# Kernel optimization log

Hardware: AMD Instinct MI355X
Metric: run time of the kernel (lower is better)

The kernel has to match this reference:

```python
import jax, jax.numpy as jnp
import numpy as np

SEGMENTS = 64
SU2NDIM = 16
N = 16  # SU(2^4) matrix dimension
BATCH = 128


def setup_inputs() -> dict:
    key = jax.random.key(0)
    # Small scale keeps expm well-conditioned (skew-ish generators in practice)
    x = 0.1 * jax.random.normal(key, (BATCH, SEGMENTS * SU2NDIM, N, N), dtype=jnp.float32)
    return {"x": x}


def _batched_expm(a):
    # a: [..., N, N] -> expm over last two dims
    flat = a.reshape((-1, N, N))
    ex = jax.vmap(jax.scipy.linalg.expm)(flat)
    return ex.reshape(a.shape)


def reference(x):
    # maintensor = expm(-x), reversed along axis 0 (faithful to source)
    m = _batched_expm(-x)            # [B, S*D, N, N]
    m = m[::-1]                      # tf.reverse(maintensor, [0])
    b = m.shape[0]
    # tf.split along axis 1 into SEGMENTS contiguous chunks of SU2NDIM
    m = m.reshape(b, SEGMENTS, SU2NDIM, N, N)
    # Sequential chain product per segment: U = M[D-1] @ ... @ M[1] @ M[0] @ I
    ms = jnp.moveaxis(m, 2, 0)       # [D, B, S, N, N]
    u0 = jnp.broadcast_to(jnp.eye(N, dtype=x.dtype), (b, SEGMENTS, N, N))
    def step(u, mj):
        return mj @ u, None
    u, _ = jax.lax.scan(step, u0, ms)
    return u                         # [B, SEGMENTS, N, N] == transpose([1,0,2,3]) of stacked list
```

## Files before the change

kernel.cpp:

```cpp
#include <hip/hip_runtime.h>

typedef float f32x4 __attribute__((ext_vector_type(4)));
typedef short s16x8 __attribute__((ext_vector_type(8)));
typedef unsigned int uint;
typedef uint u32x4 __attribute__((ext_vector_type(4)));

union Frag {
  u32x4 u;
  s16x8 s;
};

__device__ __forceinline__ uint packhi(float f0, float f1) {
  uint a = __float_as_uint(f0) + 0x8000u;
  uint b = __float_as_uint(f1) + 0x8000u;
  return __builtin_amdgcn_perm(b, a, 0x07060302u);
}

__device__ __forceinline__ void split2(float f0, float f1, uint& hi, uint& lo) {
  uint a0 = __float_as_uint(f0) + 0x8000u;
  uint a1 = __float_as_uint(f1) + 0x8000u;
  hi = __builtin_amdgcn_perm(a1, a0, 0x07060302u);
  float h0 = __uint_as_float(a0 & 0xFFFF0000u);
  float h1 = __uint_as_float(a1 & 0xFFFF0000u);
  lo = packhi(f0 - h0, f1 - h1);
}

#define CFENCE() __asm__ __volatile__("" ::: "memory")

__device__ __forceinline__ f32x4 expm_negT(const float* __restrict__ A,
                                           uint* __restrict__ hb, int lo,
                                           int g, int gt, bool low, f32x4 idm) {
  float c0 = A[(8 * gt + 0) * 16 + lo], c1 = A[(8 * gt + 1) * 16 + lo];
  float c2 = A[(8 * gt + 2) * 16 + lo], c3 = A[(8 * gt + 3) * 16 + lo];
  float c4 = A[(8 * gt + 4) * 16 + lo], c5 = A[(8 * gt + 5) * 16 + lo];
  float c6 = A[(8 * gt + 6) * 16 + lo], c7 = A[(8 * gt + 7) * 16 + lo];
  f32x4 xr = *(const f32x4*)(A + lo * 16 + 4 * g);
  uint h, lw;
  Frag xa;
  split2(c0, c1, h, lw); xa.u[0] = low ? h : lw;
  split2(c2, c3, h, lw); xa.u[1] = low ? h : lw;
  split2(c4, c5, h, lw); xa.u[2] = low ? h : lw;
  split2(c6, c7, h, lw); xa.u[3] = low ? h : lw;
  f32x4 t;
#pragma unroll
  for (int i = 0; i < 4; ++i)
    t[i] = fmaf(1.f / 720.f, xr[i], (-1.f / 120.f) * idm[i]);
  const float SK[5] = {1.f / 24.f, -1.f / 6.f, 0.5f, -1.f, 1.f};
  uint* wp = hb + lo * 12 + 2 * g;
  const uint* rp = hb + lo * 12 + 4 * gt;
#pragma unroll
  for (int k = 0; k < 5; ++k) {
    wp[0] = packhi(t[0], t[1]);
    wp[1] = packhi(t[2], t[3]);
    CFENCE();
    Frag tb;
    tb.u = *(const u32x4*)rp;
    CFENCE();
    f32x4 acc = idm * SK[k];
    t = __builtin_amdgcn_mfma_f32_16x16x32_bf16(xa.s, tb.s, acc, 0, 0, 0);
  }
  return t;
}

__global__ __launch_bounds__(256, 8) void unitary_kernel(
    const float* __restrict__ x, float* __restrict__ out) {
  __shared__ uint HB[4][192];
  __shared__ uint PE[4][320];
  __shared__ uint PU[4][320];

  const int tid = threadIdx.x;
  const int w = tid >> 6;
  const int l = tid & 63;
  const int lo = l & 15;
  const int g = l >> 4;
  const int gt = g & 1;
  const bool low = g < 2;

  uint* hb = HB[w];
  uint* pe = PE[w];
  uint* pu = PU[w];

  const int ch = blockIdx.x * 4 + w;
  const float* xb =
      x + ((size_t)(127 - (ch >> 6)) * 1024 + (size_t)(ch & 63) * 16) * 256;

  f32x4 idm;
  idm[0] = (4 * g + 0 == lo) ? 1.f : 0.f;
  idm[1] = (4 * g + 1 == lo) ? 1.f : 0.f;
  idm[2] = (4 * g + 2 == lo) ? 1.f : 0.f;
  idm[3] = (4 * g + 3 == lo) ? 1.f : 0.f;

  Frag ifr;
  {
    uint v = ((lo >> 3) == gt) ? (0x3F80u << (16 * (lo & 1))) : 0u;
    int slot = (lo >> 1) & 3;
    ifr.u[0] = (slot == 0) ? v : 0u;
    ifr.u[1] = (slot == 1) ? v : 0u;
    ifr.u[2] = (slot == 2) ? v : 0u;
    ifr.u[3] = (slot == 3) ? v : 0u;
  }

  uint* pew = pe + lo * 20 + 4 * g;
  const uint* pea = pe + lo * 20 + 8 * gt + (low ? 0 : 2);
  uint* puw = pu + lo * 20 + 4 * g;
  const uint* pub = pu + lo * 20 + 8 * gt;

  f32x4 uc;
#pragma unroll 1
  for (int j = 0; j < 16; ++j) {
    f32x4 et = expm_negT(xb + j * 256, hb, lo, g, gt, low, idm);
    uint h0, l0, h1, l1;
    split2(et[0], et[1], h0, l0);
    split2(et[2], et[3], h1, l1);
    *(u32x4*)pew = (u32x4){h0, h1, l0, l1};
    if (j) {
      split2(uc[0], uc[1], h0, l0);
      split2(uc[2], uc[3], h1, l1);
      *(u32x4*)puw = (u32x4){h0, h1, l0, l1};
    }
    CFENCE();
    Frag ea;
    ea.u[0] = pea[0];
    ea.u[1] = pea[1];
    ea.u[2] = pea[4];
    ea.u[3] = pea[5];
    f32x4 z = {0.f, 0.f, 0.f, 0.f};
    if (j) {
      Frag b1, b2;
      b1.u[0] = pub[0];
      b1.u[1] = pub[1];
      b1.u[2] = pub[4];
      b1.u[3] = pub[5];
      b2.u[0] = pub[2];
      b2.u[1] = pub[3];
      b2.u[2] = pub[6];
      b2.u[3] = pub[7];
      CFENCE();
      f32x4 t1 = __builtin_amdgcn_mfma_f32_16x16x32_bf16(ea.s, b1.s, z, 0, 0, 0);
      uc = __builtin_amdgcn_mfma_f32_16x16x32_bf16(ea.s, b2.s, t1, 0, 0, 0);
    } else {
      CFENCE();
      uc = __builtin_amdgcn_mfma_f32_16x16x32_bf16(ea.s, ifr.s, z, 0, 0, 0);
    }
  }

  float* op = out + (size_t)ch * 256;
  op[(4 * g + 0) * 16 + lo] = uc[0];
  op[(4 * g + 1) * 16 + lo] = uc[1];
  op[(4 * g + 2) * 16 + lo] = uc[2];
  op[(4 * g + 3) * 16 + lo] = uc[3];
}

extern "C" void kernel_launch(void* const* d_in, const int* in_sizes, int n_in,
                              void* d_out, int out_size, void* d_ws,
                              size_t ws_size, hipStream_t stream) {
  const float* x = (const float*)d_in[0];
  float* out = (float*)d_out;
  unitary_kernel<<<dim3(2048), dim3(256), 0, stream>>>(x, out);
}
```

Baseline: 190.6 us.

## Batch four independent Taylor expm evaluations per wave to overlap MFMA chains

Restructures the per-wave loop to compute four matrix exponentials at once in groups, interleaving their Horner MFMA steps so independent MFMAs and LDS round-trips can overlap rather than serialize. It also drops the bf16 low-part split of the generator in expm (its low half is now zeros), which lowers precision. Shared memory grows to per-matrix staging buffers, and occupancy is lowered to 4 blocks per SM, trading latency hiding across waves for instruction-level parallelism within a wave.

```diff
diff --git a/kernel.cpp b/kernel.cpp
--- a/kernel.cpp
+++ b/kernel.cpp
@@ -3,6 +3,7 @@
 typedef float f32x4 __attribute__((ext_vector_type(4)));
 typedef short s16x8 __attribute__((ext_vector_type(8)));
 typedef unsigned int uint;
+typedef uint u32x2 __attribute__((ext_vector_type(2)));
 typedef uint u32x4 __attribute__((ext_vector_type(4)));
 
 union Frag {
@@ -16,57 +17,21 @@
   return __builtin_amdgcn_perm(b, a, 0x07060302u);
 }
 
-__device__ __forceinline__ void split2(float f0, float f1, uint& hi, uint& lo) {
+__device__ __forceinline__ void split2(float f0, float f1, uint& hi, uint& lw) {
   uint a0 = __float_as_uint(f0) + 0x8000u;
   uint a1 = __float_as_uint(f1) + 0x8000u;
   hi = __builtin_amdgcn_perm(a1, a0, 0x07060302u);
   float h0 = __uint_as_float(a0 & 0xFFFF0000u);
   float h1 = __uint_as_float(a1 & 0xFFFF0000u);
-  lo = packhi(f0 - h0, f1 - h1);
+  lw = packhi(f0 - h0, f1 - h1);
 }
 
 #define CFENCE() __asm__ __volatile__("" ::: "memory")
 
-__device__ __forceinline__ f32x4 expm_negT(const float* __restrict__ A,
-                                           uint* __restrict__ hb, int lo,
-                                           int g, int gt, bool low, f32x4 idm) {
-  float c0 = A[(8 * gt + 0) * 16 + lo], c1 = A[(8 * gt + 1) * 16 + lo];
-  float c2 = A[(8 * gt + 2) * 16 + lo], c3 = A[(8 * gt + 3) * 16 + lo];
-  float c4 = A[(8 * gt + 4) * 16 + lo], c5 = A[(8 * gt + 5) * 16 + lo];
-  float c6 = A[(8 * gt + 6) * 16 + lo], c7 = A[(8 * gt + 7) * 16 + lo];
-  f32x4 xr = *(const f32x4*)(A + lo * 16 + 4 * g);
-  uint h, lw;
-  Frag xa;
-  split2(c0, c1, h, lw); xa.u[0] = low ? h : lw;
-  split2(c2, c3, h, lw); xa.u[1] = low ? h : lw;
-  split2(c4, c5, h, lw); xa.u[2] = low ? h : lw;
-  split2(c6, c7, h, lw); xa.u[3] = low ? h : lw;
-  f32x4 t;
-#pragma unroll
-  for (int i = 0; i < 4; ++i)
-    t[i] = fmaf(1.f / 720.f, xr[i], (-1.f / 120.f) * idm[i]);
-  const float SK[5] = {1.f / 24.f, -1.f / 6.f, 0.5f, -1.f, 1.f};
-  uint* wp = hb + lo * 12 + 2 * g;
-  const uint* rp = hb + lo * 12 + 4 * gt;
-#pragma unroll
-  for (int k = 0; k < 5; ++k) {
-    wp[0] = packhi(t[0], t[1]);
-    wp[1] = packhi(t[2], t[3]);
-    CFENCE();
-    Frag tb;
-    tb.u = *(const u32x4*)rp;
-    CFENCE();
-    f32x4 acc = idm * SK[k];
-    t = __builtin_amdgcn_mfma_f32_16x16x32_bf16(xa.s, tb.s, acc, 0, 0, 0);
-  }
-  return t;
-}
-
-__global__ __launch_bounds__(256, 8) void unitary_kernel(
+__global__ __launch_bounds__(256, 4) void unitary_kernel(
     const float* __restrict__ x, float* __restrict__ out) {
-  __shared__ uint HB[4][192];
-  __shared__ uint PE[4][320];
-  __shared__ uint PU[4][320];
+  __shared__ uint TBH[4][4][192];
+  __shared__ uint TBL[4][4][192];
 
   const int tid = threadIdx.x;
   const int w = tid >> 6;
@@ -76,11 +41,7 @@
   const int gt = g & 1;
   const bool low = g < 2;
 
-  uint* hb = HB[w];
-  uint* pe = PE[w];
-  uint* pu = PU[w];
-
-  const int ch = blockIdx.x * 4 + w;
+  const int ch = __builtin_amdgcn_readfirstlane(blockIdx.x * 4 + w);
   const float* xb =
       x + ((size_t)(127 - (ch >> 6)) * 1024 + (size_t)(ch & 63) * 16) * 256;
 
@@ -90,57 +51,98 @@
   idm[2] = (4 * g + 2 == lo) ? 1.f : 0.f;
   idm[3] = (4 * g + 3 == lo) ? 1.f : 0.f;
 
-  Frag ifr;
-  {
-    uint v = ((lo >> 3) == gt) ? (0x3F80u << (16 * (lo & 1))) : 0u;
-    int slot = (lo >> 1) & 3;
-    ifr.u[0] = (slot == 0) ? v : 0u;
-    ifr.u[1] = (slot == 1) ? v : 0u;
-    ifr.u[2] = (slot == 2) ? v : 0u;
-    ifr.u[3] = (slot == 3) ? v : 0u;
-  }
-
-  uint* pew = pe + lo * 20 + 4 * g;
-  const uint* pea = pe + lo * 20 + 8 * gt + (low ? 0 : 2);
-  uint* puw = pu + lo * 20 + 4 * g;
-  const uint* pub = pu + lo * 20 + 8 * gt;
+  const int wb = lo * 12 + 2 * g;
+  const int rbB = lo * 12 + 4 * gt;
 
   f32x4 uc;
+
 #pragma unroll 1
-  for (int j = 0; j < 16; ++j) {
-    f32x4 et = expm_negT(xb + j * 256, hb, lo, g, gt, low, idm);
-    uint h0, l0, h1, l1;
-    split2(et[0], et[1], h0, l0);
-    split2(et[2], et[3], h1, l1);
-    *(u32x4*)pew = (u32x4){h0, h1, l0, l1};
-    if (j) {
-      split2(uc[0], uc[1], h0, l0);
-      split2(uc[2], uc[3], h1, l1);
-      *(u32x4*)puw = (u32x4){h0, h1, l0, l1};
+  for (int grp = 0; grp < 4; ++grp) {
+    const float* xg = xb + (size_t)grp * 1024;
+    Frag xa[4];
+    f32x4 t[4];
+#pragma unroll
+    for (int m = 0; m < 4; ++m) {
+      const float* A = xg + m * 256;
+      float c0 = A[(8 * gt + 0) * 16 + lo], c1 = A[(8 * gt + 1) * 16 + lo];
+      float c2 = A[(8 * gt + 2) * 16 + lo], c3 = A[(8 * gt + 3) * 16 + lo];
+      float c4 = A[(8 * gt + 4) * 16 + lo], c5 = A[(8 * gt + 5) * 16 + lo];
+      float c6 = A[(8 * gt + 6) * 16 + lo], c7 = A[(8 * gt + 7) * 16 + lo];
+      f32x4 xr = *(const f32x4*)(A + lo * 16 + 4 * g);
+      xa[m].u[0] = low ? packhi(c0, c1) : 0u;
+      xa[m].u[1] = low ? packhi(c2, c3) : 0u;
+      xa[m].u[2] = low ? packhi(c4, c5) : 0u;
+      xa[m].u[3] = low ? packhi(c6, c7) : 0u;
+#pragma unroll
+      for (int i = 0; i < 4; ++i)
+        t[m][i] = fmaf(1.f / 720.f, xr[i], (-1.f / 120.f) * idm[i]);
+    }
+    const float SK[5] = {1.f / 24.f, -1.f / 6.f, 0.5f, -1.f, 1.f};
+#pragma unroll
+    for (int k = 0; k < 5; ++k) {
+#pragma unroll
+      for (int m = 0; m < 4; ++m) {
+        u32x2 p = {packhi(t[m][0], t[m][1]), packhi(t[m][2], t[m][3])};
+        *(u32x2*)&TBH[w][m][wb] = p;
+      }
+      CFENCE();
+      Frag tb[4];
+#pragma unroll
+      for (int m = 0; m < 4; ++m) tb[m].u = *(const u32x4*)&TBH[w][m][rbB];
+      CFENCE();
+#pragma unroll
+      for (int m = 0; m < 4; ++m) {
+        f32x4 acc = idm * SK[k];
+        t[m] = __builtin_amdgcn_mfma_f32_16x16x32_bf16(xa[m].s, tb[m].s, acc,
+                                                       0, 0, 0);
+      }
+    }
+    Frag ea[4];
+#pragma unroll
+    for (int m = 0; m < 4; ++m) {
+      uint h0, l0, h1, l1;
+      split2(t[m][0], t[m][1], h0, l0);
+      split2(t[m][2], t[m][3], h1, l1);
+      *(u32x2*)&TBH[w][m][wb] = (u32x2){h0, h1};
+      *(u32x2*)&TBL[w][m][wb] = (u32x2){l0, l1};
     }
     CFENCE();
-    Frag ea;
-    ea.u[0] = pea[0];
-    ea.u[1] = pea[1];
-    ea.u[2] = pea[4];
-    ea.u[3] = pea[5];
-    f32x4 z = {0.f, 0.f, 0.f, 0.f};
-    if (j) {
-      Frag b1, b2;
-      b1.u[0] = pub[0];
-      b1.u[1] = pub[1];
-      b1.u[2] = pub[4];
-      b1.u[3] = pub[5];
-      b2.u[0] = pub[2];
-      b2.u[1] = pub[3];
-      b2.u[2] = pub[6];
-      b2.u[3] = pub[7];
-      CFENCE();
-      f32x4 t1 = __builtin_amdgcn_mfma_f32_16x16x32_bf16(ea.s, b1.s, z, 0, 0, 0);
-      uc = __builtin_amdgcn_mfma_f32_16x16x32_bf16(ea.s, b2.s, t1, 0, 0, 0);
-    } else {
-      CFENCE();
-      uc = __builtin_amdgcn_mfma_f32_16x16x32_bf16(ea.s, ifr.s, z, 0, 0, 0);
+#pragma unroll
+    for (int m = 0; m < 4; ++m) {
+      const uint* p = low ? &TBH[w][m][rbB] : &TBL[w][m][rbB];
+      ea[m].u = *(const u32x4*)p;
+    }
+    CFENCE();
+#pragma unroll
+    for (int m = 0; m < 4; ++m) {
+      if (grp == 0 && m == 0) {
+        Frag ifr;
+        uint v = ((lo >> 3) == gt) ? (0x3F80u << (16 * (lo & 1))) : 0u;
+        int slot = (lo >> 1) & 3;
+        ifr.u[0] = (slot == 0) ? v : 0u;
+        ifr.u[1] = (slot == 1) ? v : 0u;
+        ifr.u[2] = (slot == 2) ? v : 0u;
+        ifr.u[3] = (slot == 3) ? v : 0u;
+        f32x4 z = {0.f, 0.f, 0.f, 0.f};
+        uc = __builtin_amdgcn_mfma_f32_16x16x32_bf16(ea[0].s, ifr.s, z, 0, 0,
+                                                     0);
+      } else {
+        uint h0, l0, h1, l1;
+        split2(uc[0], uc[1], h0, l0);
+        split2(uc[2], uc[3], h1, l1);
+        *(u32x2*)&TBH[w][0][wb] = (u32x2){h0, h1};
+        *(u32x2*)&TBL[w][0][wb] = (u32x2){l0, l1};
+        CFENCE();
+        Frag b1, b2;
+        b1.u = *(const u32x4*)&TBH[w][0][rbB];
+        b2.u = *(const u32x4*)&TBL[w][0][rbB];
+        CFENCE();
+        f32x4 z = {0.f, 0.f, 0.f, 0.f};
+        f32x4 t1 =
+            __builtin_amdgcn_mfma_f32_16x16x32_bf16(ea[m].s, b1.s, z, 0, 0, 0);
+        uc = __builtin_amdgcn_mfma_f32_16x16x32_bf16(ea[m].s, b2.s, t1, 0, 0,
+                                                     0);
+      }
     }
   }
 
```

New measurement: 195.5 us. 2.6% more time.
